# Optimization experiments

Hardware: AMD Instinct MI355X
Metric: run time of the kernel (lower is better)

Reference implementation:

```python
import jax, jax.numpy as jnp
import numpy as np

B, T, D, H = 8, 2048, 1024, 128  # batch, seq (== block_size), n_embd, head_size


def setup_inputs() -> dict:
    key = jax.random.key(0)
    kx, kq, kk, kv = jax.random.split(key, 4)
    s = D ** -0.5  # rough linear-init scale
    return {
        "x": jax.random.normal(kx, (B, T, D), dtype=jnp.float32),
        "Wq": jax.random.normal(kq, (D, H), dtype=jnp.float32) * s,
        "Wk": jax.random.normal(kk, (D, H), dtype=jnp.float32) * s,
        "Wv": jax.random.normal(kv, (D, H), dtype=jnp.float32) * s,
    }


def reference(x, Wq, Wk, Wv):
    # Linear projections (no bias)
    q = x @ Wq  # [B, T, H]
    k = x @ Wk  # [B, T, H]
    v = x @ Wv  # [B, T, H]
    scale = k.shape[-1] ** -0.5
    scores = jnp.einsum("bth,bsh->bts", q, k) * scale  # [B, T, T]
    # causal mask from tril buffer
    causal = jnp.tril(jnp.ones((T, T), dtype=bool))
    scores = jnp.where(causal, scores, jnp.finfo(scores.dtype).min)
    att = jax.nn.softmax(scores, axis=-1)
    out = jnp.einsum("bts,bsh->bth", att, v)  # [B, T, H]
    return out
```

## Files before the change

### kernel.cpp

```cpp
#include <hip/hip_runtime.h>
#include <hip/hip_bf16.h>
#include <stdint.h>

typedef float f32x4 __attribute__((ext_vector_type(4)));
typedef __bf16 bf16x8 __attribute__((ext_vector_type(8)));

#define T_SEQ 2048
#define D_EMB 1024
#define H_DIM 128
#define NBATCH 8
#define NTOK 16384

typedef __attribute__((address_space(3))) uint32_t lds_u32;
typedef const __attribute__((address_space(1))) uint32_t glb_u32;

#define DPPF(x, ctrl)                                                    \
  __int_as_float(__builtin_amdgcn_update_dpp(                            \
      0, __float_as_int(x), (ctrl), 0xF, 0xF, true))

#define PIPE_FENCE()                                       \
  do {                                                     \
    asm volatile("s_waitcnt vmcnt(0)" ::: "memory");       \
    __builtin_amdgcn_s_barrier();                          \
    __builtin_amdgcn_sched_barrier(0);                     \
  } while (0)


__global__ __launch_bounds__(256) void prep_w_kernel(
    const float* __restrict__ Wq, const float* __restrict__ Wk,
    const float* __restrict__ Wv, __hip_bfloat16* __restrict__ Wt) {
  const int mat = blockIdx.x >> 7;
  const int h = blockIdx.x & 127;
  const float* W = (mat == 0) ? Wq : ((mat == 1) ? Wk : Wv);
  __hip_bfloat16* dst = Wt + (size_t)(mat * 128 + h) * D_EMB;
  for (int k = threadIdx.x; k < D_EMB; k += 256)
    dst[k] = __float2bfloat16(W[(size_t)k * H_DIM + h]);
}

__global__ __launch_bounds__(256) void proj_kernel(
    const float* __restrict__ x, const __hip_bfloat16* __restrict__ Wt,
    __hip_bfloat16* __restrict__ qb, __hip_bfloat16* __restrict__ kb,
    __hip_bfloat16* __restrict__ vt) {
  __shared__ __align__(16) float Af[128 * 64];
  __shared__ __align__(16) __hip_bfloat16 Bs[128 * 64];
  const int tid = threadIdx.x;
  const int wave = tid >> 6;
  const int lane = tid & 63;
  const int g = lane >> 4;
  const int lr = lane & 15;
  const int ntile = blockIdx.x % 3;
  const int mtile = blockIdx.x / 3;
  const int m0 = mtile * 128;
  const int wm = (wave >> 1) * 64;
  const int wn = (wave & 1) * 64;
  const __hip_bfloat16* WtT = Wt + (size_t)ntile * 128 * D_EMB;
  const float* xA = x + (size_t)m0 * D_EMB;

  f32x4 acc[4][4];
#pragma unroll
  for (int m = 0; m < 4; ++m)
#pragma unroll
    for (int n = 0; n < 4; ++n) acc[m][n] = f32x4{0.f, 0.f, 0.f, 0.f};

  auto stage = [&](int k0) {
#pragma unroll
    for (int i = 0; i < 8; ++i) {
      const int e = i * 256 + tid;
      const int row = e >> 4;
      const int un = e & 15;
      __builtin_amdgcn_global_load_lds(
          (glb_u32*)(uintptr_t)(xA + (size_t)row * D_EMB + k0 +
                                ((un ^ (row & 15)) * 4)),
          (lds_u32*)(uintptr_t)(&Af[e * 4]), 16, 0, 0);
    }
#pragma unroll
    for (int i = 0; i < 4; ++i) {
      const int u = i * 256 + tid;
      const int row = u >> 3;
      const int chunk = u & 7;
      __builtin_amdgcn_global_load_lds(
          (glb_u32*)(uintptr_t)(WtT + (size_t)row * D_EMB + k0 +
                                ((chunk ^ (row & 7)) * 8)),
          (lds_u32*)(uintptr_t)(&Bs[row * 64 + chunk * 8]), 16, 0, 0);
    }
  };

  auto compute = [&]() {
#pragma unroll
    for (int kk = 0; kk < 2; ++kk) {
      bf16x8 a[4];
#pragma unroll
      for (int m = 0; m < 4; ++m) {
        const int row = wm + m * 16 + lr;
        const int u0 = kk * 8 + g * 2;
        const f32x4 lo = *reinterpret_cast<const f32x4*>(
            &Af[row * 64 + ((u0 ^ (row & 15)) * 4)]);
        const f32x4 hi = *reinterpret_cast<const f32x4*>(
            &Af[row * 64 + (((u0 + 1) ^ (row & 15)) * 4)]);
        union { bf16x8 v; __hip_bfloat16 h[8]; } u;
        u.h[0] = __float2bfloat16(lo[0]);
        u.h[1] = __float2bfloat16(lo[1]);
        u.h[2] = __float2bfloat16(lo[2]);
        u.h[3] = __float2bfloat16(lo[3]);
        u.h[4] = __float2bfloat16(hi[0]);
        u.h[5] = __float2bfloat16(hi[1]);
        u.h[6] = __float2bfloat16(hi[2]);
        u.h[7] = __float2bfloat16(hi[3]);
        a[m] = u.v;
      }
#pragma unroll
      for (int n = 0; n < 4; ++n) {
        const int col = wn + n * 16 + lr;
        bf16x8 b = *reinterpret_cast<const bf16x8*>(
            &Bs[col * 64 + (((kk * 4 + g) ^ (col & 7)) * 8)]);
#pragma unroll
        for (int m = 0; m < 4; ++m)
          acc[m][n] =
              __builtin_amdgcn_mfma_f32_16x16x32_bf16(a[m], b, acc[m][n], 0, 0, 0);
      }
    }
  };

  for (int k = 0; k < 16; ++k) {
    __syncthreads();
    stage(k * 64);
    __syncthreads();
    compute();
  }

#pragma unroll
  for (int n = 0; n < 4; ++n) {
    const int ng = ntile * 128 + wn + n * 16 + lr;
    const int head = ng >> 7;
    const int h = ng & 127;
#pragma unroll
    for (int m = 0; m < 4; ++m) {
#pragma unroll
      for (int r = 0; r < 4; ++r) {
        const int row = m0 + wm + m * 16 + g * 4 + r;
        const __hip_bfloat16 val = __float2bfloat16(acc[m][n][r]);
        if (head == 0) {
          qb[(size_t)row * H_DIM + h] = val;
        } else if (head == 1) {
          kb[(size_t)row * H_DIM + h] = val;
        } else {
          const int bi = row >> 11;
          const int t = row & (T_SEQ - 1);
          vt[((size_t)bi * H_DIM + h) * T_SEQ + t] = val;
        }
      }
    }
  }
}

__global__ __launch_bounds__(512) void attn_kernel(
    const __hip_bfloat16* __restrict__ qb, const __hip_bfloat16* __restrict__ kb,
    const __hip_bfloat16* __restrict__ vt, float* __restrict__ out,
    float* __restrict__ PA_O, float* __restrict__ PA_ml,
    float* __restrict__ PB_O, float* __restrict__ PB_ml) {
  __shared__ __align__(16) __hip_bfloat16 KV[2][16384];
  __shared__ __align__(16) __hip_bfloat16 Pl[8][16][40];
  __shared__ float Obuf[4][16][132];
  __shared__ float mbuf[8][16];
  __shared__ float lbuf[8][16];

  const int tid = threadIdx.x;
  const int wave = tid >> 6;
  const int lane = tid & 63;
  const int g = lane >> 4;
  const int lr = lane & 15;
  const int qt = wave >> 1;
  const int kp = wave & 1;
  const int idx = blockIdx.x;
  const int b = idx & 7;
  const int u = idx >> 3;

  const __hip_bfloat16* qB = qb + (size_t)b * T_SEQ * H_DIM;
  const __hip_bfloat16* kB = kb + (size_t)b * T_SEQ * H_DIM;
  const __hip_bfloat16* vB = vt + (size_t)b * H_DIM * T_SEQ;
  const float scale = 0.08838834764831845f;

  auto stage = [&](__hip_bfloat16* buf, int s0) {
#pragma unroll
    for (int i = 0; i < 2; ++i) {
      const int uu = tid + i * 512;
      const int row = uu >> 4, grp = uu & 15;
      __builtin_amdgcn_global_load_lds(
          (glb_u32*)(uintptr_t)(kB + (size_t)(s0 + row) * H_DIM +
                                ((grp ^ (row & 15)) * 8)),
          (lds_u32*)(uintptr_t)(buf + uu * 8), 16, 0, 0);
    }
#pragma unroll
    for (int i = 0; i < 2; ++i) {
      const int uu = tid + i * 512;
      const int h = uu >> 3, grp = uu & 7;
      __builtin_amdgcn_global_load_lds(
          (glb_u32*)(uintptr_t)(vB + (size_t)h * T_SEQ + s0 +
                                ((grp ^ (h & 7)) * 8)),
          (lds_u32*)(uintptr_t)(buf + 8192 + uu * 8), 16, 0, 0);
    }
  };

  auto process = [&](int tile, int rr0, int rr1, int mode) {
    const int qrow0 = tile * 64 + qt * 16;
    bf16x8 qf[4];
#pragma unroll
    for (int kt = 0; kt < 4; ++kt)
      qf[kt] = *reinterpret_cast<const bf16x8*>(
          qB + (size_t)(qrow0 + lr) * H_DIM + kt * 32 + g * 8);

    f32x4 oacc[8];
#pragma unroll
    for (int i = 0; i < 8; ++i) oacc[i] = f32x4{0.f, 0.f, 0.f, 0.f};
    float mrow[4] = {-1e30f, -1e30f, -1e30f, -1e30f};
    float lrow[4] = {0.f, 0.f, 0.f, 0.f};

    __hip_bfloat16* bufA = &KV[0][0];
    __hip_bfloat16* bufB = &KV[1][0];
    stage(bufA, rr0 * 64);

    for (int r = rr0; r <= rr1; ++r) {
      PIPE_FENCE();
      if (r < rr1) stage(bufB, (r + 1) * 64);
      const int s0 = r * 64;
      const bool active = (s0 + kp * 32) <= (qrow0 + 15);
      if (active) {
        f32x4 sacc[2];
        sacc[0] = f32x4{0.f, 0.f, 0.f, 0.f};
        sacc[1] = f32x4{0.f, 0.f, 0.f, 0.f};
#pragma unroll
        for (int nt = 0; nt < 2; ++nt) {
          const int kl = kp * 32 + nt * 16 + lr;
          const __hip_bfloat16* kr = bufA + kl * 128;
#pragma unroll
          for (int kt = 0; kt < 4; ++kt) {
            bf16x8 kf = *reinterpret_cast<const bf16x8*>(
                kr + (((kt * 4 + g) ^ (kl & 15)) * 8));
            sacc[nt] = __builtin_amdgcn_mfma_f32_16x16x32_bf16(qf[kt], kf,
                                                               sacc[nt], 0, 0, 0);
          }
        }
        bf16x8 vf[8];
#pragma unroll
        for (int ht = 0; ht < 8; ++ht) {
          const int h = ht * 16 + lr;
          vf[ht] = *reinterpret_cast<const bf16x8*>(
              bufA + 8192 + h * 64 + (((kp * 4 + g) ^ (h & 7)) * 8));
        }
        float sv[2][4];
#pragma unroll
        for (int nt = 0; nt < 2; ++nt)
#pragma unroll
          for (int rr = 0; rr < 4; ++rr) {
            const int key = s0 + kp * 32 + nt * 16 + lr;
            const int qr = qrow0 + g * 4 + rr;
            const float s = sacc[nt][rr] * scale;
            sv[nt][rr] = (key > qr) ? -1e30f : s;
          }
        float pm[4];
#pragma unroll
        for (int rr = 0; rr < 4; ++rr) pm[rr] = fmaxf(sv[0][rr], sv[1][rr]);
#pragma unroll
        for (int rr = 0; rr < 4; ++rr) {
          pm[rr] = fmaxf(pm[rr], DPPF(pm[rr], 0xB1));
          pm[rr] = fmaxf(pm[rr], DPPF(pm[rr], 0x4E));
          pm[rr] = fmaxf(pm[rr], DPPF(pm[rr], 0x141));
          pm[rr] = fmaxf(pm[rr], DPPF(pm[rr], 0x140));
        }
        bool ok = true;
#pragma unroll
        for (int rr = 0; rr < 4; ++rr) ok = ok && (pm[rr] <= mrow[rr] + 8.f);
        if (!__all((int)ok)) {
#pragma unroll
          for (int rr = 0; rr < 4; ++rr) {
            const float mnew = fmaxf(mrow[rr], pm[rr]);
            const float corr = __expf(mrow[rr] - mnew);
            mrow[rr] = mnew;
            lrow[rr] *= corr;
#pragma unroll
            for (int ht = 0; ht < 8; ++ht) oacc[ht][rr] *= corr;
          }
        }
        float rs[4];
#pragma unroll
        for (int rr = 0; rr < 4; ++rr) {
          const float p0 = __expf(sv[0][rr] - mrow[rr]);
          const float p1 = __expf(sv[1][rr] - mrow[rr]);
          Pl[wave][g * 4 + rr][lr] = __float2bfloat16(p0);
          Pl[wave][g * 4 + rr][16 + lr] = __float2bfloat16(p1);
          rs[rr] = p0 + p1;
        }
#pragma unroll
        for (int rr = 0; rr < 4; ++rr) {
          rs[rr] += DPPF(rs[rr], 0xB1);
          rs[rr] += DPPF(rs[rr], 0x4E);
          rs[rr] += DPPF(rs[rr], 0x141);
          rs[rr] += DPPF(rs[rr], 0x140);
        }
#pragma unroll
        for (int rr = 0; rr < 4; ++rr) lrow[rr] += rs[rr];
        bf16x8 pf = *reinterpret_cast<const bf16x8*>(&Pl[wave][lr][g * 8]);
#pragma unroll
        for (int ht = 0; ht < 8; ++ht)
          oacc[ht] = __builtin_amdgcn_mfma_f32_16x16x32_bf16(pf, vf[ht],
                                                             oacc[ht], 0, 0, 0);
      }
      __hip_bfloat16* t = bufA; bufA = bufB; bufB = t;
    }

    __syncthreads();
    if (kp == 1) {
#pragma unroll
      for (int ht = 0; ht < 8; ++ht)
#pragma unroll
        for (int rr = 0; rr < 4; ++rr)
          Obuf[qt][g * 4 + rr][ht * 16 + lr] = oacc[ht][rr];
      if (lr == 0) {
#pragma unroll
        for (int rr = 0; rr < 4; ++rr) {
          mbuf[wave][g * 4 + rr] = mrow[rr];
          lbuf[wave][g * 4 + rr] = lrow[rr];
        }
      }
    }
    __syncthreads();
    if (kp == 0) {
#pragma unroll
      for (int rr = 0; rr < 4; ++rr) {
        const float mB = mbuf[wave + 1][g * 4 + rr];
        const float lB = lbuf[wave + 1][g * 4 + rr];
        const float M = fmaxf(mrow[rr], mB);
        const float a = __expf(mrow[rr] - M);
        const float bt = __expf(mB - M);
        lrow[rr] = a * lrow[rr] + bt * lB;
        mrow[rr] = M;
#pragma unroll
        for (int ht = 0; ht < 8; ++ht)
          oacc[ht][rr] =
              a * oacc[ht][rr] + bt * Obuf[qt][g * 4 + rr][ht * 16 + lr];
      }
      if (mode == 0) {
#pragma unroll
        for (int ht = 0; ht < 8; ++ht)
#pragma unroll
          for (int rr = 0; rr < 4; ++rr) {
            const int qr = qrow0 + g * 4 + rr;
            out[((size_t)b * T_SEQ + qr) * H_DIM + ht * 16 + lr] =
                oacc[ht][rr] / lrow[rr];
          }
      } else {
        float* PO = (mode == 1) ? PA_O : PB_O;
        float* Pm = (mode == 1) ? PA_ml : PB_ml;
        const int slot = tile - 16;
#pragma unroll
        for (int rr = 0; rr < 4; ++rr) {
          const size_t pr = (size_t)(b * 16 + slot) * 64 + qt * 16 + g * 4 + rr;
#pragma unroll
          for (int ht = 0; ht < 8; ++ht)
            PO[pr * 128 + ht * 16 + lr] = oacc[ht][rr];
          if (lr == 0) {
            Pm[pr * 2 + 0] = mrow[rr];
            Pm[pr * 2 + 1] = lrow[rr];
          }
        }
      }
    }
    __syncthreads();
  };

  if (u < 16) {
    process(u, 0, u, 0);
    process(31 - u, 0, 15 - u, 1);
  } else {
    const int v = u - 16;
    process(31 - v, 16 - v, 31 - v, 2);
  }
}

__global__ __launch_bounds__(256) void combine_kernel(
    const float* __restrict__ PA_O, const float* __restrict__ PA_ml,
    const float* __restrict__ PB_O, const float* __restrict__ PB_ml,
    float* __restrict__ out) {
  const int b = blockIdx.x >> 4;
  const int s = blockIdx.x & 15;
  const int tid = threadIdx.x;
  const int row = tid >> 2;
  const int c0 = (tid & 3) * 32;
  const size_t pr = (size_t)(b * 16 + s) * 64 + row;
  const float mA = PA_ml[pr * 2], lA = PA_ml[pr * 2 + 1];
  const float mB = PB_ml[pr * 2], lB = PB_ml[pr * 2 + 1];
  const float M = fmaxf(mA, mB);
  const float a = __expf(mA - M), bb = __expf(mB - M);
  const float inv = 1.f / (a * lA + bb * lB);
  const float* oa = PA_O + pr * 128 + c0;
  const float* ob = PB_O + pr * 128 + c0;
  float* op = out + ((size_t)b * T_SEQ + (16 + s) * 64 + row) * H_DIM + c0;
#pragma unroll
  for (int i = 0; i < 32; i += 4) {
    const float4 x = *reinterpret_cast<const float4*>(oa + i);
    const float4 y = *reinterpret_cast<const float4*>(ob + i);
    float4 z;
    z.x = (a * x.x + bb * y.x) * inv;
    z.y = (a * x.y + bb * y.y) * inv;
    z.z = (a * x.z + bb * y.z) * inv;
    z.w = (a * x.w + bb * y.w) * inv;
    *reinterpret_cast<float4*>(op + i) = z;
  }
}

extern "C" void kernel_launch(void* const* d_in, const int* in_sizes, int n_in,
                              void* d_out, int out_size, void* d_ws, size_t ws_size,
                              hipStream_t stream) {
  const float* x = (const float*)d_in[0];
  const float* Wq = (const float*)d_in[1];
  const float* Wk = (const float*)d_in[2];
  const float* Wv = (const float*)d_in[3];
  float* out = (float*)d_out;

  __hip_bfloat16* Wt = (__hip_bfloat16*)d_ws;
  __hip_bfloat16* qbuf = Wt + (size_t)3 * 128 * 1024;
  __hip_bfloat16* kbuf = qbuf + (size_t)NTOK * H_DIM;
  __hip_bfloat16* vbuf = kbuf + (size_t)NTOK * H_DIM;
  float* fbase = (float*)(vbuf + (size_t)NBATCH * H_DIM * T_SEQ);
  float* PA_O = fbase;
  float* PA_ml = PA_O + (size_t)1048576;
  float* PB_O = PA_ml + 16384;
  float* PB_ml = PB_O + (size_t)1048576;

  hipLaunchKernelGGL(prep_w_kernel, dim3(384), dim3(256), 0, stream, Wq, Wk, Wv, Wt);
  hipLaunchKernelGGL(proj_kernel, dim3(384), dim3(256), 0, stream, x, Wt, qbuf,
                     kbuf, vbuf);
  hipLaunchKernelGGL(attn_kernel, dim3(256), dim3(512), 0, stream, qbuf, kbuf,
                     vbuf, out, PA_O, PA_ml, PB_O, PB_ml);
  hipLaunchKernelGGL(combine_kernel, dim3(128), dim3(256), 0, stream, PA_O,
                     PA_ml, PB_O, PB_ml, out);
}
```

Measured before the change: 86.67 us.

## Convert x to bf16 once at staging and retile projection into 96-wide N tiles

The projection GEMM now loads x through registers, converts it to bf16 a single time, and stores it to swizzled LDS. Previously each wave re-converted the fp32 values from LDS on every fragment read. The N dimension is split into four 96-column tiles, so the grid grows from 384 to 512 blocks, which fills more CUs and halves A-tile LDS usage. In exchange, x loads no longer use direct-to-LDS and go through VGPRs, and each block does less MFMA work per staged A tile.

```diff
diff --git a/kernel.cpp b/kernel.cpp
--- a/kernel.cpp
+++ b/kernel.cpp
@@ -41,75 +41,78 @@
     const float* __restrict__ x, const __hip_bfloat16* __restrict__ Wt,
     __hip_bfloat16* __restrict__ qb, __hip_bfloat16* __restrict__ kb,
     __hip_bfloat16* __restrict__ vt) {
-  __shared__ __align__(16) float Af[128 * 64];
-  __shared__ __align__(16) __hip_bfloat16 Bs[128 * 64];
+  __shared__ __align__(16) __hip_bfloat16 As[128 * 64];
+  __shared__ __align__(16) __hip_bfloat16 Bs[96 * 64];
   const int tid = threadIdx.x;
   const int wave = tid >> 6;
   const int lane = tid & 63;
   const int g = lane >> 4;
   const int lr = lane & 15;
-  const int ntile = blockIdx.x % 3;
-  const int mtile = blockIdx.x / 3;
+  const int mtile = blockIdx.x >> 2;
+  const int nq = blockIdx.x & 3;
   const int m0 = mtile * 128;
   const int wm = (wave >> 1) * 64;
-  const int wn = (wave & 1) * 64;
-  const __hip_bfloat16* WtT = Wt + (size_t)ntile * 128 * D_EMB;
+  const int wn = (wave & 1) * 48;
+  const __hip_bfloat16* WtT = Wt + (size_t)nq * 96 * D_EMB;
   const float* xA = x + (size_t)m0 * D_EMB;
 
-  f32x4 acc[4][4];
+  f32x4 acc[4][3];
 #pragma unroll
   for (int m = 0; m < 4; ++m)
 #pragma unroll
-    for (int n = 0; n < 4; ++n) acc[m][n] = f32x4{0.f, 0.f, 0.f, 0.f};
-
-  auto stage = [&](int k0) {
-#pragma unroll
-    for (int i = 0; i < 8; ++i) {
-      const int e = i * 256 + tid;
-      const int row = e >> 4;
-      const int un = e & 15;
-      __builtin_amdgcn_global_load_lds(
-          (glb_u32*)(uintptr_t)(xA + (size_t)row * D_EMB + k0 +
-                                ((un ^ (row & 15)) * 4)),
-          (lds_u32*)(uintptr_t)(&Af[e * 4]), 16, 0, 0);
-    }
-#pragma unroll
-    for (int i = 0; i < 4; ++i) {
+    for (int n = 0; n < 3; ++n) acc[m][n] = f32x4{0.f, 0.f, 0.f, 0.f};
+
+  const int arow0 = tid >> 3;
+  const int achunk = tid & 7;
+
+  for (int k = 0; k < 16; ++k) {
+    const int k0 = k * 64;
+    __syncthreads();
+
+    float4 fa[4][2];
+#pragma unroll
+    for (int p = 0; p < 4; ++p) {
+      const float* src = xA + (size_t)(arow0 + p * 32) * D_EMB + k0 + achunk * 8;
+      fa[p][0] = *reinterpret_cast<const float4*>(src);
+      fa[p][1] = *reinterpret_cast<const float4*>(src + 4);
+    }
+#pragma unroll
+    for (int i = 0; i < 3; ++i) {
       const int u = i * 256 + tid;
-      const int row = u >> 3;
-      const int chunk = u & 7;
+      const int row = u >> 3, chunk = u & 7;
       __builtin_amdgcn_global_load_lds(
           (glb_u32*)(uintptr_t)(WtT + (size_t)row * D_EMB + k0 +
                                 ((chunk ^ (row & 7)) * 8)),
           (lds_u32*)(uintptr_t)(&Bs[row * 64 + chunk * 8]), 16, 0, 0);
     }
-  };
-
-  auto compute = [&]() {
+#pragma unroll
+    for (int p = 0; p < 4; ++p) {
+      const int row = arow0 + p * 32;
+      union { bf16x8 v; __hip_bfloat16 h[8]; } u;
+      u.h[0] = __float2bfloat16(fa[p][0].x);
+      u.h[1] = __float2bfloat16(fa[p][0].y);
+      u.h[2] = __float2bfloat16(fa[p][0].z);
+      u.h[3] = __float2bfloat16(fa[p][0].w);
+      u.h[4] = __float2bfloat16(fa[p][1].x);
+      u.h[5] = __float2bfloat16(fa[p][1].y);
+      u.h[6] = __float2bfloat16(fa[p][1].z);
+      u.h[7] = __float2bfloat16(fa[p][1].w);
+      *reinterpret_cast<bf16x8*>(
+          &As[row * 64 + ((achunk ^ (row & 7)) * 8)]) = u.v;
+    }
+    __syncthreads();
+
 #pragma unroll
     for (int kk = 0; kk < 2; ++kk) {
       bf16x8 a[4];
 #pragma unroll
       for (int m = 0; m < 4; ++m) {
         const int row = wm + m * 16 + lr;
-        const int u0 = kk * 8 + g * 2;
-        const f32x4 lo = *reinterpret_cast<const f32x4*>(
-            &Af[row * 64 + ((u0 ^ (row & 15)) * 4)]);
-        const f32x4 hi = *reinterpret_cast<const f32x4*>(
-            &Af[row * 64 + (((u0 + 1) ^ (row & 15)) * 4)]);
-        union { bf16x8 v; __hip_bfloat16 h[8]; } u;
-        u.h[0] = __float2bfloat16(lo[0]);
-        u.h[1] = __float2bfloat16(lo[1]);
-        u.h[2] = __float2bfloat16(lo[2]);
-        u.h[3] = __float2bfloat16(lo[3]);
-        u.h[4] = __float2bfloat16(hi[0]);
-        u.h[5] = __float2bfloat16(hi[1]);
-        u.h[6] = __float2bfloat16(hi[2]);
-        u.h[7] = __float2bfloat16(hi[3]);
-        a[m] = u.v;
-      }
-#pragma unroll
-      for (int n = 0; n < 4; ++n) {
+        a[m] = *reinterpret_cast<const bf16x8*>(
+            &As[row * 64 + (((kk * 4 + g) ^ (row & 7)) * 8)]);
+      }
+#pragma unroll
+      for (int n = 0; n < 3; ++n) {
         const int col = wn + n * 16 + lr;
         bf16x8 b = *reinterpret_cast<const bf16x8*>(
             &Bs[col * 64 + (((kk * 4 + g) ^ (col & 7)) * 8)]);
@@ -119,18 +122,11 @@
               __builtin_amdgcn_mfma_f32_16x16x32_bf16(a[m], b, acc[m][n], 0, 0, 0);
       }
     }
-  };
-
-  for (int k = 0; k < 16; ++k) {
-    __syncthreads();
-    stage(k * 64);
-    __syncthreads();
-    compute();
   }
 
 #pragma unroll
-  for (int n = 0; n < 4; ++n) {
-    const int ng = ntile * 128 + wn + n * 16 + lr;
+  for (int n = 0; n < 3; ++n) {
+    const int ng = nq * 96 + wn + n * 16 + lr;
     const int head = ng >> 7;
     const int h = ng & 127;
 #pragma unroll
@@ -428,7 +424,7 @@
   float* PB_ml = PB_O + (size_t)1048576;
 
   hipLaunchKernelGGL(prep_w_kernel, dim3(384), dim3(256), 0, stream, Wq, Wk, Wv, Wt);
-  hipLaunchKernelGGL(proj_kernel, dim3(384), dim3(256), 0, stream, x, Wt, qbuf,
+  hipLaunchKernelGGL(proj_kernel, dim3(512), dim3(256), 0, stream, x, Wt, qbuf,
                      kbuf, vbuf);
   hipLaunchKernelGGL(attn_kernel, dim3(256), dim3(512), 0, stream, qbuf, kbuf,
                      vbuf, out, PA_O, PA_ml, PB_O, PB_ml);
```

Result: slower. 94.79 us (+9.4%).
